# Kernel optimization log

Measured on AMD Instinct MI355X. Metric: run time of the kernel, lower is better.

Reference implementation:

```python
import jax, jax.numpy as jnp
import numpy as np

B, S, D_IN, D_OUT, R = 8, 2048, 2048, 2048, 16

def setup_inputs() -> dict:
    key = jax.random.key(0)
    k = jax.random.split(key, 5)
    scale_w = 1.0 / np.sqrt(D_IN)
    return {
        "x": jax.random.normal(k[0], (B, S, D_IN), dtype=jnp.float32),
        "A_params": jax.random.normal(k[1], (B, D_OUT, R), dtype=jnp.float32) * 0.02,
        "B_params": jax.random.normal(k[2], (B, R, D_IN), dtype=jnp.float32) * 0.02,
        "W": jax.random.normal(k[3], (D_OUT, D_IN), dtype=jnp.float32) * scale_w,
        "b": jax.random.normal(k[4], (D_OUT,), dtype=jnp.float32) * scale_w,
    }

def reference(x, A_params, B_params, W, b):
    # base: x @ W^T + b  -> [B, S, out]
    base_out = jnp.einsum("bsi,oi->bso", x, W) + b
    # intermediate = x @ B^T -> [B, S, r]
    intermediate = jnp.einsum("bsi,bri->bsr", x, B_params)
    # adaptation = intermediate @ A^T -> [B, S, out]
    adaptation = jnp.einsum("bsr,bor->bso", intermediate, A_params)
    return base_out + adaptation
```

## Files before the change

### kernel.cpp

```cpp
#include <hip/hip_runtime.h>
#include <cstdint>
#include <cstddef>

typedef __attribute__((ext_vector_type(4))) float  floatx4;
typedef __attribute__((ext_vector_type(8))) __bf16 bf16x8;
typedef __attribute__((ext_vector_type(8))) unsigned short u16x8;

#define M_TOT 16384
#define N_TOT 2048
#define K_TOT 2048
#define NBATCH 8
#define RLORA 16
#define NT 32

__device__ __forceinline__ unsigned short f32_to_bf16(float f) {
  unsigned u = __float_as_uint(f);
  u += 0x7fffu + ((u >> 16) & 1u);
  return (unsigned short)(u >> 16);
}

#define GLOAD_LDS16(gp, lp)                                                        \
  __builtin_amdgcn_global_load_lds((__attribute__((address_space(1))) void*)(void*)(gp), \
                                   (__attribute__((address_space(3))) void*)(void*)(lp), \
                                   16, 0, 0)

template<int V> struct IC { static constexpr int value = V; };

__global__ void k_convert(const float* __restrict__ in, unsigned short* __restrict__ out, int n8) {
  int i = blockIdx.x * blockDim.x + threadIdx.x;
  if (i >= n8) return;
  const float4* p = (const float4*)in + (size_t)i * 2;
  float4 v0 = p[0], v1 = p[1];
  u16x8 o;
  o[0] = f32_to_bf16(v0.x); o[1] = f32_to_bf16(v0.y);
  o[2] = f32_to_bf16(v0.z); o[3] = f32_to_bf16(v0.w);
  o[4] = f32_to_bf16(v1.x); o[5] = f32_to_bf16(v1.y);
  o[6] = f32_to_bf16(v1.z); o[7] = f32_to_bf16(v1.w);
  *(u16x8*)(out + (size_t)i * 8) = o;
}

__global__ void k_convert_a(const float* __restrict__ A, unsigned short* __restrict__ abf) {
  int row = blockIdx.x * blockDim.x + threadIdx.x;
  if (row >= NBATCH * N_TOT) return;
  const float4* p = (const float4*)(A + (size_t)row * RLORA);
  float4 v0 = p[0], v1 = p[1], v2 = p[2], v3 = p[3];
  u16x8 lo, hi2, z = {0,0,0,0,0,0,0,0};
  lo[0] = f32_to_bf16(v0.x); lo[1] = f32_to_bf16(v0.y);
  lo[2] = f32_to_bf16(v0.z); lo[3] = f32_to_bf16(v0.w);
  lo[4] = f32_to_bf16(v1.x); lo[5] = f32_to_bf16(v1.y);
  lo[6] = f32_to_bf16(v1.z); lo[7] = f32_to_bf16(v1.w);
  hi2[0] = f32_to_bf16(v2.x); hi2[1] = f32_to_bf16(v2.y);
  hi2[2] = f32_to_bf16(v2.z); hi2[3] = f32_to_bf16(v2.w);
  hi2[4] = f32_to_bf16(v3.x); hi2[5] = f32_to_bf16(v3.y);
  hi2[6] = f32_to_bf16(v3.z); hi2[7] = f32_to_bf16(v3.w);
  u16x8* dst = (u16x8*)(abf + (size_t)row * 32);
  dst[0] = lo; dst[1] = hi2; dst[2] = z; dst[3] = z;
}

__global__ __launch_bounds__(256) void k_inter(const unsigned short* __restrict__ xbf,
                                               const unsigned short* __restrict__ bpbf,
                                               unsigned short* __restrict__ interbf) {
  const int tid  = threadIdx.x;
  const int lane = tid & 63;
  const int wv   = tid >> 6;
  const int l15  = lane & 15;
  const int hi   = lane >> 4;
  const int m0   = blockIdx.x * 64;
  const int bb   = m0 >> 11;

  floatx4 zero = {0.f, 0.f, 0.f, 0.f};
  floatx4 acc[4] = {zero, zero, zero, zero};

  const unsigned short* bpb = bpbf + (size_t)bb * (RLORA * K_TOT);
  const int kb0 = wv * 512;
  for (int kb = kb0; kb < kb0 + 512; kb += 32) {
    bf16x8 bfr = *(const bf16x8*)(bpb + (size_t)l15 * K_TOT + kb + hi * 8);
    #pragma unroll
    for (int mi = 0; mi < 4; ++mi) {
      bf16x8 afr = *(const bf16x8*)(xbf + (size_t)(m0 + mi * 16 + l15) * K_TOT + kb + hi * 8);
      acc[mi] = __builtin_amdgcn_mfma_f32_16x16x32_bf16(afr, bfr, acc[mi], 0, 0, 0);
    }
  }

  __shared__ floatx4 red[4][4][64];
  #pragma unroll
  for (int mi = 0; mi < 4; ++mi) red[wv][mi][lane] = acc[mi];
  __syncthreads();
  if (wv == 0) {
    #pragma unroll
    for (int mi = 0; mi < 4; ++mi) {
      floatx4 s = red[0][mi][lane] + red[1][mi][lane] + red[2][mi][lane] + red[3][mi][lane];
      #pragma unroll
      for (int j = 0; j < 4; ++j) {
        int m = m0 + mi * 16 + hi * 4 + j;
        interbf[(size_t)m * 32 + l15] = f32_to_bf16(s[j]);
        interbf[(size_t)m * 32 + 16 + l15] = 0;
      }
    }
  }
}

#define STAGE_A(bufi, h, tt) do {                                                      \
  GLOAD_LDS16(Ag + (h)*262144 + (tt)*64 + gOff0, AsB + ((bufi)*2+(h))*16384 + ldsB0);  \
  GLOAD_LDS16(Ag + (h)*262144 + (tt)*64 + gOff1, AsB + ((bufi)*2+(h))*16384 + ldsB1);  \
} while(0)
#define STAGE_B(bufi, h, tt) do {                                                      \
  GLOAD_LDS16(Bg + (h)*262144 + (tt)*64 + gOff0, BsB + ((bufi)*2+(h))*16384 + ldsB0);  \
  GLOAD_LDS16(Bg + (h)*262144 + (tt)*64 + gOff1, BsB + ((bufi)*2+(h))*16384 + ldsB1);  \
} while(0)
#define LDA(bufi, qm, mi, ks) (*(const bf16x8*)(AsB + ((bufi)*2 + wm)*16384 + \
  ((qm)*64 + (mi)*16 + l15)*128 + ((((ks)*4 + hi) ^ swz) * 16)))
#define LDB(bufi, ni, ks)     (*(const bf16x8*)(BsB + ((bufi)*2 + (wn>>1))*16384 + \
  (((wn&1)*64 + (ni)*16 + l15)*128 + ((((ks)*4 + hi) ^ swz) * 16))))

__global__ __launch_bounds__(512, 2) void k_gemm(const unsigned short* __restrict__ xbf,
                                                 const unsigned short* __restrict__ wbf,
                                                 const unsigned short* __restrict__ interbf,
                                                 const unsigned short* __restrict__ abf,
                                                 const float* __restrict__ bias,
                                                 float* __restrict__ out) {
  __shared__ unsigned short As[2][2][8192];
  __shared__ unsigned short Bs[2][2][8192];
  const int tid  = threadIdx.x;
  const int lane = tid & 63;
  const int wid  = tid >> 6;
  const int wm   = wid >> 2;
  const int wn   = wid & 3;
  const int l15  = lane & 15;
  const int hi   = lane >> 4;
  const int swz  = l15 & 7;

  int bid  = blockIdx.x;
  int swzb = ((bid & 7) << 6) | (bid >> 3);
  const int mt = swzb >> 3;
  const int nt = swzb & 7;
  const int mrow0 = mt << 8;
  const int ncol0 = nt << 8;
  const int bb = mrow0 >> 11;

  const int m0 = mrow0 + wm * 128;
  const int n0 = ncol0 + wn * 64;

  const unsigned short* Ag = xbf + (size_t)mrow0 * K_TOT;
  const unsigned short* Bg = wbf + (size_t)ncol0 * K_TOT;
  char* AsB = (char*)As;
  char* BsB = (char*)Bs;

  const int r0    = tid >> 3;
  const int k80   = (tid & 7) ^ (r0 & 7);
  const int gOff0 = r0 * K_TOT + k80 * 8;
  const int gOff1 = gOff0 + 64 * K_TOT;
  const int ldsB0 = wid * 1024;
  const int ldsB1 = 8192 + wid * 1024;

  floatx4 acc[8][4];
  {
    bf16x8 la[8], lb[4];
    #pragma unroll
    for (int mi = 0; mi < 8; ++mi)
      la[mi] = *(const bf16x8*)(interbf + (size_t)(m0 + mi * 16 + l15) * 32 + hi * 8);
    #pragma unroll
    for (int ni = 0; ni < 4; ++ni)
      lb[ni] = *(const bf16x8*)(abf + ((size_t)bb * N_TOT + n0 + ni * 16 + l15) * 32 + hi * 8);

    STAGE_B(0, 0, 0); STAGE_B(0, 1, 0); STAGE_A(0, 0, 0); STAGE_A(0, 1, 0);
    STAGE_B(1, 0, 1); STAGE_B(1, 1, 1); STAGE_A(1, 0, 1);

    floatx4 z = {0.f, 0.f, 0.f, 0.f};
    #pragma unroll
    for (int mi = 0; mi < 8; ++mi)
      #pragma unroll
      for (int ni = 0; ni < 4; ++ni)
        acc[mi][ni] = __builtin_amdgcn_mfma_f32_16x16x32_bf16(la[mi], lb[ni], z, 0, 0, 0);
  }
  asm volatile("s_waitcnt vmcnt(6)" ::: "memory");
  __builtin_amdgcn_s_barrier();

  auto tile = [&](int t, auto s1_, auto s2_, auto vm_) {
    constexpr int S1 = decltype(s1_)::value;
    constexpr int S2 = decltype(s2_)::value;
    constexpr int VM = decltype(vm_)::value;
    const int buf = t & 1;
    bf16x8 af[4][2], bfr[4][2];

    #pragma unroll
    for (int mi = 0; mi < 4; ++mi) { af[mi][0] = LDA(buf, 0, mi, 0); af[mi][1] = LDA(buf, 0, mi, 1); }
    #pragma unroll
    for (int ni = 0; ni < 2; ++ni) { bfr[ni][0] = LDB(buf, ni, 0); bfr[ni][1] = LDB(buf, ni, 1); }
    if constexpr (S1) STAGE_A(buf ^ 1, 1, t + 1);
    __builtin_amdgcn_s_barrier();
    asm volatile("s_waitcnt lgkmcnt(0)" ::: "memory");
    __builtin_amdgcn_s_setprio(1);
    #pragma unroll
    for (int mi = 0; mi < 4; ++mi)
      #pragma unroll
      for (int ni = 0; ni < 2; ++ni) {
        acc[mi][ni] = __builtin_amdgcn_mfma_f32_16x16x32_bf16(af[mi][0], bfr[ni][0], acc[mi][ni], 0, 0, 0);
        acc[mi][ni] = __builtin_amdgcn_mfma_f32_16x16x32_bf16(af[mi][1], bfr[ni][1], acc[mi][ni], 0, 0, 0);
      }
    __builtin_amdgcn_s_setprio(0);
    __builtin_amdgcn_s_barrier();

    #pragma unroll
    for (int ni = 0; ni < 2; ++ni) { bfr[2+ni][0] = LDB(buf, 2+ni, 0); bfr[2+ni][1] = LDB(buf, 2+ni, 1); }
    __builtin_amdgcn_s_barrier();
    asm volatile("s_waitcnt lgkmcnt(0)" ::: "memory");
    __builtin_amdgcn_s_setprio(1);
    #pragma unroll
    for (int mi = 0; mi < 4; ++mi)
      #pragma unroll
      for (int ni = 0; ni < 2; ++ni) {
        acc[mi][2+ni] = __builtin_amdgcn_mfma_f32_16x16x32_bf16(af[mi][0], bfr[2+ni][0], acc[mi][2+ni], 0, 0, 0);
        acc[mi][2+ni] = __builtin_amdgcn_mfma_f32_16x16x32_bf16(af[mi][1], bfr[2+ni][1], acc[mi][2+ni], 0, 0, 0);
      }
    __builtin_amdgcn_s_setprio(0);
    __builtin_amdgcn_s_barrier();

    #pragma unroll
    for (int mi = 0; mi < 4; ++mi) { af[mi][0] = LDA(buf, 1, mi, 0); af[mi][1] = LDA(buf, 1, mi, 1); }
    if constexpr (S2) { STAGE_B(buf, 0, t + 2); STAGE_B(buf, 1, t + 2); }
    __builtin_amdgcn_s_barrier();
    asm volatile("s_waitcnt lgkmcnt(0)" ::: "memory");
    __builtin_amdgcn_s_setprio(1);
    #pragma unroll
    for (int mi = 0; mi < 4; ++mi)
      #pragma unroll
      for (int ni = 0; ni < 2; ++ni) {
        acc[4+mi][ni] = __builtin_amdgcn_mfma_f32_16x16x32_bf16(af[mi][0], bfr[ni][0], acc[4+mi][ni], 0, 0, 0);
        acc[4+mi][ni] = __builtin_amdgcn_mfma_f32_16x16x32_bf16(af[mi][1], bfr[ni][1], acc[4+mi][ni], 0, 0, 0);
      }
    __builtin_amdgcn_s_setprio(0);
    __builtin_amdgcn_s_barrier();

    if constexpr (S2) STAGE_A(buf, 0, t + 2);
    __builtin_amdgcn_s_barrier();
    asm volatile("s_waitcnt lgkmcnt(0)" ::: "memory");
    __builtin_amdgcn_s_setprio(1);
    #pragma unroll
    for (int mi = 0; mi < 4; ++mi)
      #pragma unroll
      for (int ni = 0; ni < 2; ++ni) {
        acc[4+mi][2+ni] = __builtin_amdgcn_mfma_f32_16x16x32_bf16(af[mi][0], bfr[2+ni][0], acc[4+mi][2+ni], 0, 0, 0);
        acc[4+mi][2+ni] = __builtin_amdgcn_mfma_f32_16x16x32_bf16(af[mi][1], bfr[2+ni][1], acc[4+mi][2+ni], 0, 0, 0);
      }
    __builtin_amdgcn_s_setprio(0);
    if constexpr (VM == 6)      asm volatile("s_waitcnt vmcnt(6)" ::: "memory");
    else if constexpr (VM == 0) asm volatile("s_waitcnt vmcnt(0)" ::: "memory");
    __builtin_amdgcn_s_barrier();
  };

  for (int t = 0; t < NT - 2; ++t) tile(t, IC<1>{}, IC<1>{}, IC<6>{});
  tile(NT - 2, IC<1>{}, IC<0>{}, IC<0>{});
  tile(NT - 1, IC<0>{}, IC<0>{}, IC<-1>{});

  #pragma unroll
  for (int ni = 0; ni < 4; ++ni) {
    int col = n0 + ni * 16 + l15;
    float bv = bias[col];
    #pragma unroll
    for (int mi = 0; mi < 8; ++mi) {
      int r = m0 + mi * 16 + hi * 4;
      #pragma unroll
      for (int j = 0; j < 4; ++j)
        out[(size_t)(r + j) * N_TOT + col] = acc[mi][ni][j] + bv;
    }
  }
}

extern "C" void kernel_launch(void* const* d_in, const int* in_sizes, int n_in,
                              void* d_out, int out_size, void* d_ws, size_t ws_size,
                              hipStream_t stream) {
  const float* x    = (const float*)d_in[0];
  const float* Ap   = (const float*)d_in[1];
  const float* Bp   = (const float*)d_in[2];
  const float* W    = (const float*)d_in[3];
  const float* bias = (const float*)d_in[4];
  float* out = (float*)d_out;

  char* ws = (char*)d_ws;
  unsigned short* xbf     = (unsigned short*)(ws);
  unsigned short* wbf     = (unsigned short*)(ws + 67108864);
  unsigned short* abf     = (unsigned short*)(ws + 67108864 + 8388608);
  unsigned short* bpbf    = (unsigned short*)(ws + 67108864 + 8388608 + 1048576);
  unsigned short* interbf = (unsigned short*)(ws + 67108864 + 8388608 + 1048576 + 524288);

  k_convert<<<dim3(16384), dim3(256), 0, stream>>>(x,  xbf,  4194304);
  k_convert<<<dim3(2048),  dim3(256), 0, stream>>>(W,  wbf,   524288);
  k_convert<<<dim3(128),   dim3(256), 0, stream>>>(Bp, bpbf,   32768);
  k_convert_a<<<dim3(64),  dim3(256), 0, stream>>>(Ap, abf);

  k_inter<<<dim3(256), dim3(256), 0, stream>>>(xbf, bpbf, interbf);

  k_gemm<<<dim3(512), dim3(512), 0, stream>>>(xbf, wbf, interbf, abf, bias, out);
}
```

Before: 210.0 us.

## Software-pipeline LDS fragment reads across MFMA phases with ping-pong registers

Restructures the per-tile schedule so the LDS reads for the next quadrant, and for the next tile's first A/B fragments, are issued before the current MFMA batch. Partial lgkmcnt waits replace the full drains. Fragment registers are double-buffered (afA/afB, bfP/bfQ), the loop is unrolled by two with compile-time buffer indices, and LDS addresses are precomputed into base offsets. The aim is to hide LDS read latency behind matrix-core work and cut address arithmetic. The cost is higher register pressure under a 2-waves-per-SIMD launch bound, plus changed vmcnt thresholds that must still keep the global-to-LDS loads safely ordered.

```diff
diff --git a/kernel.cpp b/kernel.cpp
--- a/kernel.cpp
+++ b/kernel.cpp
@@ -108,10 +108,19 @@
   GLOAD_LDS16(Bg + (h)*262144 + (tt)*64 + gOff0, BsB + ((bufi)*2+(h))*16384 + ldsB0);  \
   GLOAD_LDS16(Bg + (h)*262144 + (tt)*64 + gOff1, BsB + ((bufi)*2+(h))*16384 + ldsB1);  \
 } while(0)
-#define LDA(bufi, qm, mi, ks) (*(const bf16x8*)(AsB + ((bufi)*2 + wm)*16384 + \
-  ((qm)*64 + (mi)*16 + l15)*128 + ((((ks)*4 + hi) ^ swz) * 16)))
-#define LDB(bufi, ni, ks)     (*(const bf16x8*)(BsB + ((bufi)*2 + (wn>>1))*16384 + \
-  (((wn&1)*64 + (ni)*16 + l15)*128 + ((((ks)*4 + hi) ^ swz) * 16))))
+#define RDA_(B2, qm, mi, ks) (*(const bf16x8*)(AsB + (B2)*32768 + aBase + (qm)*8192 + (mi)*2048 + koff[ks]))
+#define RDB_(B2, ni, ks)     (*(const bf16x8*)(BsB + (B2)*32768 + bBase + (ni)*2048 + koff[ks]))
+#define BAR() __builtin_amdgcn_s_barrier()
+#define MFMA16(MB, NB, AF, BF) do {                                                        \
+  _Pragma("unroll")                                                                        \
+  for (int mi = 0; mi < 4; ++mi) {                                                         \
+    _Pragma("unroll")                                                                      \
+    for (int j = 0; j < 2; ++j) {                                                          \
+      acc[(MB)+mi][(NB)+j] = __builtin_amdgcn_mfma_f32_16x16x32_bf16(AF[mi][0], BF[j][0], acc[(MB)+mi][(NB)+j], 0, 0, 0); \
+      acc[(MB)+mi][(NB)+j] = __builtin_amdgcn_mfma_f32_16x16x32_bf16(AF[mi][1], BF[j][1], acc[(MB)+mi][(NB)+j], 0, 0, 0); \
+    }                                                                                      \
+  }                                                                                        \
+} while(0)
 
 __global__ __launch_bounds__(512, 2) void k_gemm(const unsigned short* __restrict__ xbf,
                                                  const unsigned short* __restrict__ wbf,
@@ -153,7 +162,15 @@
   const int ldsB0 = wid * 1024;
   const int ldsB1 = 8192 + wid * 1024;
 
+  const int aBase = wm * 16384 + l15 * 128;
+  const int bBase = wn * 8192  + l15 * 128;
+  int koff[2];
+  koff[0] = ((0 * 4 + hi) ^ swz) * 16;
+  koff[1] = ((1 * 4 + hi) ^ swz) * 16;
+
   floatx4 acc[8][4];
+  bf16x8 afA[4][2], afB[4][2], bfP[2][2], bfQ[2][2];
+
   {
     bf16x8 la[8], lb[4];
     #pragma unroll
@@ -174,84 +191,69 @@
         acc[mi][ni] = __builtin_amdgcn_mfma_f32_16x16x32_bf16(la[mi], lb[ni], z, 0, 0, 0);
   }
   asm volatile("s_waitcnt vmcnt(6)" ::: "memory");
-  __builtin_amdgcn_s_barrier();
-
-  auto tile = [&](int t, auto s1_, auto s2_, auto vm_) {
-    constexpr int S1 = decltype(s1_)::value;
-    constexpr int S2 = decltype(s2_)::value;
-    constexpr int VM = decltype(vm_)::value;
-    const int buf = t & 1;
-    bf16x8 af[4][2], bfr[4][2];
-
-    #pragma unroll
-    for (int mi = 0; mi < 4; ++mi) { af[mi][0] = LDA(buf, 0, mi, 0); af[mi][1] = LDA(buf, 0, mi, 1); }
-    #pragma unroll
-    for (int ni = 0; ni < 2; ++ni) { bfr[ni][0] = LDB(buf, ni, 0); bfr[ni][1] = LDB(buf, ni, 1); }
-    if constexpr (S1) STAGE_A(buf ^ 1, 1, t + 1);
-    __builtin_amdgcn_s_barrier();
+  BAR();
+  #pragma unroll
+  for (int mi = 0; mi < 4; ++mi) { afA[mi][0] = RDA_(0, 0, mi, 0); afA[mi][1] = RDA_(0, 0, mi, 1); }
+  #pragma unroll
+  for (int j = 0; j < 2; ++j)    { bfP[j][0]  = RDB_(0, j, 0);     bfP[j][1]  = RDB_(0, j, 1); }
+
+  auto tile_step = [&](int t, auto bufc, auto s1c, auto s2c, auto vmc, auto lastc,
+                       auto& bfF, auto& bfS) {
+    constexpr int BUF  = decltype(bufc)::value;
+    constexpr int S1   = decltype(s1c)::value;
+    constexpr int S2   = decltype(s2c)::value;
+    constexpr int VM   = decltype(vmc)::value;
+    constexpr int LAST = decltype(lastc)::value;
+
+    #pragma unroll
+    for (int j = 0; j < 2; ++j) { bfS[j][0] = RDB_(BUF, 2 + j, 0); bfS[j][1] = RDB_(BUF, 2 + j, 1); }
+    if constexpr (S1) STAGE_A(BUF ^ 1, 1, t + 1);
+    BAR();
+    asm volatile("s_waitcnt lgkmcnt(4)" ::: "memory");
+    __builtin_amdgcn_s_setprio(1);
+    MFMA16(0, 0, afA, bfF);
+    __builtin_amdgcn_s_setprio(0);
+    BAR();
+
+    #pragma unroll
+    for (int mi = 0; mi < 4; ++mi) { afB[mi][0] = RDA_(BUF, 1, mi, 0); afB[mi][1] = RDA_(BUF, 1, mi, 1); }
+    BAR();
+    asm volatile("s_waitcnt lgkmcnt(8)" ::: "memory");
+    __builtin_amdgcn_s_setprio(1);
+    MFMA16(0, 2, afA, bfS);
+    __builtin_amdgcn_s_setprio(0);
+    BAR();
+
+    if constexpr (S2) { STAGE_B(BUF, 0, t + 2); STAGE_B(BUF, 1, t + 2); }
+    BAR();
     asm volatile("s_waitcnt lgkmcnt(0)" ::: "memory");
     __builtin_amdgcn_s_setprio(1);
-    #pragma unroll
-    for (int mi = 0; mi < 4; ++mi)
-      #pragma unroll
-      for (int ni = 0; ni < 2; ++ni) {
-        acc[mi][ni] = __builtin_amdgcn_mfma_f32_16x16x32_bf16(af[mi][0], bfr[ni][0], acc[mi][ni], 0, 0, 0);
-        acc[mi][ni] = __builtin_amdgcn_mfma_f32_16x16x32_bf16(af[mi][1], bfr[ni][1], acc[mi][ni], 0, 0, 0);
-      }
-    __builtin_amdgcn_s_setprio(0);
-    __builtin_amdgcn_s_barrier();
-
-    #pragma unroll
-    for (int ni = 0; ni < 2; ++ni) { bfr[2+ni][0] = LDB(buf, 2+ni, 0); bfr[2+ni][1] = LDB(buf, 2+ni, 1); }
-    __builtin_amdgcn_s_barrier();
-    asm volatile("s_waitcnt lgkmcnt(0)" ::: "memory");
-    __builtin_amdgcn_s_setprio(1);
-    #pragma unroll
-    for (int mi = 0; mi < 4; ++mi)
-      #pragma unroll
-      for (int ni = 0; ni < 2; ++ni) {
-        acc[mi][2+ni] = __builtin_amdgcn_mfma_f32_16x16x32_bf16(af[mi][0], bfr[2+ni][0], acc[mi][2+ni], 0, 0, 0);
-        acc[mi][2+ni] = __builtin_amdgcn_mfma_f32_16x16x32_bf16(af[mi][1], bfr[2+ni][1], acc[mi][2+ni], 0, 0, 0);
-      }
-    __builtin_amdgcn_s_setprio(0);
-    __builtin_amdgcn_s_barrier();
-
-    #pragma unroll
-    for (int mi = 0; mi < 4; ++mi) { af[mi][0] = LDA(buf, 1, mi, 0); af[mi][1] = LDA(buf, 1, mi, 1); }
-    if constexpr (S2) { STAGE_B(buf, 0, t + 2); STAGE_B(buf, 1, t + 2); }
-    __builtin_amdgcn_s_barrier();
-    asm volatile("s_waitcnt lgkmcnt(0)" ::: "memory");
-    __builtin_amdgcn_s_setprio(1);
-    #pragma unroll
-    for (int mi = 0; mi < 4; ++mi)
-      #pragma unroll
-      for (int ni = 0; ni < 2; ++ni) {
-        acc[4+mi][ni] = __builtin_amdgcn_mfma_f32_16x16x32_bf16(af[mi][0], bfr[ni][0], acc[4+mi][ni], 0, 0, 0);
-        acc[4+mi][ni] = __builtin_amdgcn_mfma_f32_16x16x32_bf16(af[mi][1], bfr[ni][1], acc[4+mi][ni], 0, 0, 0);
-      }
-    __builtin_amdgcn_s_setprio(0);
-    __builtin_amdgcn_s_barrier();
-
-    if constexpr (S2) STAGE_A(buf, 0, t + 2);
-    __builtin_amdgcn_s_barrier();
-    asm volatile("s_waitcnt lgkmcnt(0)" ::: "memory");
-    __builtin_amdgcn_s_setprio(1);
-    #pragma unroll
-    for (int mi = 0; mi < 4; ++mi)
-      #pragma unroll
-      for (int ni = 0; ni < 2; ++ni) {
-        acc[4+mi][2+ni] = __builtin_amdgcn_mfma_f32_16x16x32_bf16(af[mi][0], bfr[2+ni][0], acc[4+mi][2+ni], 0, 0, 0);
-        acc[4+mi][2+ni] = __builtin_amdgcn_mfma_f32_16x16x32_bf16(af[mi][1], bfr[2+ni][1], acc[4+mi][2+ni], 0, 0, 0);
-      }
-    __builtin_amdgcn_s_setprio(0);
-    if constexpr (VM == 6)      asm volatile("s_waitcnt vmcnt(6)" ::: "memory");
+    MFMA16(4, 2, afB, bfS);
+    __builtin_amdgcn_s_setprio(0);
+    if constexpr (VM == 4)      asm volatile("s_waitcnt vmcnt(4)" ::: "memory");
     else if constexpr (VM == 0) asm volatile("s_waitcnt vmcnt(0)" ::: "memory");
-    __builtin_amdgcn_s_barrier();
+    BAR();
+
+    if constexpr (!LAST) {
+      #pragma unroll
+      for (int mi = 0; mi < 4; ++mi) { afA[mi][0] = RDA_(BUF ^ 1, 0, mi, 0); afA[mi][1] = RDA_(BUF ^ 1, 0, mi, 1); }
+      #pragma unroll
+      for (int j = 0; j < 2; ++j)    { bfS[j][0] = RDB_(BUF ^ 1, j, 0);      bfS[j][1] = RDB_(BUF ^ 1, j, 1); }
+    }
+    if constexpr (S2) STAGE_A(BUF, 0, t + 2);
+    BAR();
+    __builtin_amdgcn_s_setprio(1);
+    MFMA16(4, 0, afB, bfF);
+    __builtin_amdgcn_s_setprio(0);
+    BAR();
   };
 
-  for (int t = 0; t < NT - 2; ++t) tile(t, IC<1>{}, IC<1>{}, IC<6>{});
-  tile(NT - 2, IC<1>{}, IC<0>{}, IC<0>{});
-  tile(NT - 1, IC<0>{}, IC<0>{}, IC<-1>{});
+  for (int t = 0; t < NT - 2; t += 2) {
+    tile_step(t,     IC<0>{}, IC<1>{}, IC<1>{}, IC<4>{}, IC<0>{}, bfP, bfQ);
+    tile_step(t + 1, IC<1>{}, IC<1>{}, IC<1>{}, IC<4>{}, IC<0>{}, bfQ, bfP);
+  }
+  tile_step(NT - 2, IC<0>{}, IC<1>{}, IC<0>{}, IC<0>{},  IC<0>{}, bfP, bfQ);
+  tile_step(NT - 1, IC<1>{}, IC<0>{}, IC<0>{}, IC<-1>{}, IC<1>{}, bfQ, bfP);
 
   #pragma unroll
   for (int ni = 0; ni < 4; ++ni) {
```

Result: faster. 198.8 us (-5.3%).
